# Kernel tuning notes

Measured on AMD Instinct MI355X. Metric: run time of the kernel, lower is better.

The kernel has to match this reference:

```python
import jax, jax.numpy as jnp
import numpy as np

HID = 1024
INTER = 4096
NUM_EXPERTS = 4096
NUM_KEYS = 64  # floor(sqrt(4096))
TOP_K = 8
B, S = 2, 2048


def setup_inputs() -> dict:
    key = jax.random.key(0)
    ks = jax.random.split(key, 7)
    sc = 0.02
    return {
        "hidden_states": jax.random.normal(ks[0], (B, S, HID), jnp.float32),
        "w_gate": jax.random.normal(ks[1], (INTER, HID), jnp.float32) * sc,
        "w_up": jax.random.normal(ks[2], (INTER, HID), jnp.float32) * sc,
        "w_down": jax.random.normal(ks[3], (HID, INTER), jnp.float32) * sc,
        "w_router": jax.random.normal(ks[4], (NUM_KEYS * 2, HID), jnp.float32) * sc,
        "down_embed": jax.random.normal(ks[5], (NUM_EXPERTS, HID), jnp.float32) * sc,
        "up_embed": jax.random.normal(ks[6], (NUM_EXPERTS, HID), jnp.float32) * sc,
    }


def reference(hidden_states, w_gate, w_up, w_down, w_router, down_embed, up_embed):
    b, s, h = hidden_states.shape
    n = b * s
    # router: [b,s,2*nk] -> row-major reshape to (2, n, nk), matching torch .view
    router_logits = (hidden_states @ w_router.T).reshape(2, n, NUM_KEYS)
    # topk with k == nk is a full descending sort (faithful to torch .topk)
    scores_xy, idx_xy = jax.lax.top_k(router_logits, NUM_KEYS)
    scores_x, scores_y = scores_xy[0], scores_xy[1]  # (n, nk) each
    idx_x, idx_y = idx_xy[0], idx_xy[1]
    all_scores = (scores_x[:, :, None] + scores_y[:, None, :]).reshape(n, NUM_KEYS * NUM_KEYS)
    all_indices = (idx_x[:, :, None] * NUM_KEYS + idx_y[:, None, :]).reshape(n, NUM_KEYS * NUM_KEYS)
    scores, pos = jax.lax.top_k(all_scores, TOP_K)  # (n, top_k)
    indices = jnp.take_along_axis(all_indices, pos, axis=-1)
    routing_weights = jax.nn.softmax(scores, axis=-1)
    routing_weights = routing_weights / routing_weights.sum(-1, keepdims=True)  # norm_topk_prob
    de = down_embed[indices]  # (n, top_k, h)
    ue = up_embed[indices]    # (n, top_k, h)
    x_flat = hidden_states.reshape(n, h)
    ew = jnp.einsum('nkh,nh->nk', de, x_flat)
    ew = jax.nn.silu(ew) * routing_weights
    experts_states = jnp.einsum('nk,nkh->nh', ew, ue).reshape(b, s, h)
    mlp = (jax.nn.silu(x_flat @ w_gate.T) * (x_flat @ w_up.T)) @ w_down.T
    out = mlp.reshape(b, s, h) + experts_states
    return (out, router_logits)
```

## Files before the change

### kernel.cpp

```cpp
#include <hip/hip_runtime.h>
#include <hip/hip_bf16.h>
#include <stdint.h>

typedef __bf16 bf16;
typedef __attribute__((ext_vector_type(8))) __bf16 bf16x8;
typedef __attribute__((ext_vector_type(4))) float f32x4;

static constexpr int kTok = 4096;
static constexpr int kHid = 1024;
static constexpr int kInter = 4096;

#define GLDS16(g, l)                                                \
  __builtin_amdgcn_global_load_lds(                                 \
      (const __attribute__((address_space(1))) void*)(g),           \
      (__attribute__((address_space(3))) void*)(l), 16, 0, 0)

__global__ void __launch_bounds__(256) k_cvt_all(
    const float* X, const float* Wg, const float* Wu, const float* Wd,
    const float* Wr, bf16* Xb, bf16* Wgb, bf16* Wub, bf16* Wdb, bf16* Wrb) {
  const float* src;
  bf16* dst;
  long n;
  switch (blockIdx.y) {
    case 0: src = X;  dst = Xb;  n = (long)kTok * kHid;   break;
    case 1: src = Wg; dst = Wgb; n = (long)kInter * kHid; break;
    case 2: src = Wu; dst = Wub; n = (long)kInter * kHid; break;
    case 3: src = Wd; dst = Wdb; n = (long)kHid * kInter; break;
    default: src = Wr; dst = Wrb; n = 128L * kHid;        break;
  }
  const long i = ((long)blockIdx.x * 256 + threadIdx.x) * 8;
  if (i >= n) return;
  const f32x4 a = *(const f32x4*)(src + i);
  const f32x4 b = *(const f32x4*)(src + i + 4);
  bf16x8 o;
#pragma unroll
  for (int k = 0; k < 4; ++k) { o[k] = (bf16)a[k]; o[4 + k] = (bf16)b[k]; }
  *(bf16x8*)(dst + i) = o;
}

__global__ void __launch_bounds__(256, 2) gemm_router(
    const bf16* A, const bf16* Bm, float* outF) {
  constexpr int K = kHid, N = 128;
  __shared__ bf16 sA[128 * 32];
  __shared__ bf16 sB[128 * 32];
  const int t = threadIdx.x;
  const int w = t >> 6;
  const int L = t & 63;
  const long m0 = (long)blockIdx.y * 128;
  const int zb = blockIdx.z * 256;
  const int wm = (w >> 1) * 64;
  const int wn = (w & 1) * 64;

  f32x4 acc[4][4];
  const f32x4 fzero = {0.f, 0.f, 0.f, 0.f};
#pragma unroll
  for (int i = 0; i < 4; ++i)
#pragma unroll
    for (int j = 0; j < 4; ++j) acc[i][j] = fzero;

  const int r0 = t >> 2;
  const int ko = (t & 3) * 8;
  const bf16* gA0 = A + (m0 + r0) * K + zb + ko;
  const bf16* gA1 = gA0 + (long)64 * K;
  const bf16* gB0 = Bm + (long)r0 * K + zb + ko;
  const bf16* gB1 = gB0 + (long)64 * K;
  bf16* lA0 = sA + w * 512;
  bf16* lA1 = sA + 2048 + w * 512;
  bf16* lB0 = sB + w * 512;
  bf16* lB1 = sB + 2048 + w * 512;

  const int la = L & 15;
  const int lk = (L >> 4) * 8;
  const bf16* sAr = sA + (wm + la) * 32 + lk;
  const bf16* sBr = sB + (wn + la) * 32 + lk;

  for (int kt = 0; kt < 8; ++kt) {
    const int k0 = kt << 5;
    GLDS16(gA0 + k0, lA0);
    GLDS16(gA1 + k0, lA1);
    GLDS16(gB0 + k0, lB0);
    GLDS16(gB1 + k0, lB1);
    __syncthreads();
    bf16x8 af[4], bfm[4];
#pragma unroll
    for (int i = 0; i < 4; ++i) {
      af[i] = *(const bf16x8*)(sAr + i * 16 * 32);
      bfm[i] = *(const bf16x8*)(sBr + i * 16 * 32);
    }
#pragma unroll
    for (int i = 0; i < 4; ++i)
#pragma unroll
      for (int j = 0; j < 4; ++j)
        acc[i][j] = __builtin_amdgcn_mfma_f32_16x16x32_bf16(af[i], bfm[j],
                                                            acc[i][j], 0, 0, 0);
    __syncthreads();
  }
  const long col0 = wn + la;
  const long row0 = m0 + wm + (L >> 4) * 4;
#pragma unroll
  for (int i = 0; i < 4; ++i)
#pragma unroll
    for (int j = 0; j < 4; ++j)
#pragma unroll
      for (int r = 0; r < 4; ++r)
        __hip_atomic_fetch_add(&outF[(row0 + i * 16 + r) * N + col0 + j * 16],
                               acc[i][j][r], __ATOMIC_RELAXED,
                               __HIP_MEMORY_SCOPE_AGENT);
}

__global__ void __launch_bounds__(256, 2) gemm_gu(
    const bf16* X, const bf16* Wg, const bf16* Wu, bf16* H) {
  constexpr int K = kHid, N = kInter;
  __shared__ bf16 sX[128 * 32];
  __shared__ bf16 sG[128 * 32];
  __shared__ bf16 sU[128 * 32];
  const int t = threadIdx.x;
  const int w = t >> 6;
  const int L = t & 63;
  const long m0 = (long)blockIdx.y * 128;
  const long n0 = (long)blockIdx.x * 128;
  const int wm = (w >> 1) * 64;
  const int wn = (w & 1) * 64;

  f32x4 accG[4][4], accU[4][4];
  const f32x4 fzero = {0.f, 0.f, 0.f, 0.f};
#pragma unroll
  for (int i = 0; i < 4; ++i)
#pragma unroll
    for (int j = 0; j < 4; ++j) { accG[i][j] = fzero; accU[i][j] = fzero; }

  const int r0 = t >> 2;
  const int ko = (t & 3) * 8;
  const bf16* gX0 = X + (m0 + r0) * K + ko;
  const bf16* gX1 = gX0 + (long)64 * K;
  const bf16* gG0 = Wg + (n0 + r0) * K + ko;
  const bf16* gG1 = gG0 + (long)64 * K;
  const bf16* gU0 = Wu + (n0 + r0) * K + ko;
  const bf16* gU1 = gU0 + (long)64 * K;
  bf16* lX0 = sX + w * 512;
  bf16* lX1 = sX + 2048 + w * 512;
  bf16* lG0 = sG + w * 512;
  bf16* lG1 = sG + 2048 + w * 512;
  bf16* lU0 = sU + w * 512;
  bf16* lU1 = sU + 2048 + w * 512;

  const int la = L & 15;
  const int lk = (L >> 4) * 8;
  const bf16* sXr = sX + (wm + la) * 32 + lk;
  const bf16* sGr = sG + (wn + la) * 32 + lk;
  const bf16* sUr = sU + (wn + la) * 32 + lk;

  for (int kt = 0; kt < K / 32; ++kt) {
    const int k0 = kt << 5;
    GLDS16(gX0 + k0, lX0);
    GLDS16(gX1 + k0, lX1);
    GLDS16(gG0 + k0, lG0);
    GLDS16(gG1 + k0, lG1);
    GLDS16(gU0 + k0, lU0);
    GLDS16(gU1 + k0, lU1);
    __syncthreads();
    bf16x8 af[4], bg[4], bu[4];
#pragma unroll
    for (int i = 0; i < 4; ++i) {
      af[i] = *(const bf16x8*)(sXr + i * 16 * 32);
      bg[i] = *(const bf16x8*)(sGr + i * 16 * 32);
      bu[i] = *(const bf16x8*)(sUr + i * 16 * 32);
    }
#pragma unroll
    for (int i = 0; i < 4; ++i)
#pragma unroll
      for (int j = 0; j < 4; ++j) {
        accG[i][j] = __builtin_amdgcn_mfma_f32_16x16x32_bf16(af[i], bg[j],
                                                             accG[i][j], 0, 0, 0);
        accU[i][j] = __builtin_amdgcn_mfma_f32_16x16x32_bf16(af[i], bu[j],
                                                             accU[i][j], 0, 0, 0);
      }
    __syncthreads();
  }
  const long col0 = n0 + wn + la;
  const long row0 = m0 + wm + (L >> 4) * 4;
#pragma unroll
  for (int i = 0; i < 4; ++i)
#pragma unroll
    for (int j = 0; j < 4; ++j)
#pragma unroll
      for (int r = 0; r < 4; ++r) {
        const float g = accG[i][j][r];
        const float u = accU[i][j][r];
        H[(row0 + i * 16 + r) * N + col0 + j * 16] =
            (bf16)(g / (1.f + __expf(-g)) * u);
      }
}

__global__ void __launch_bounds__(256, 2) gemm_down(
    const bf16* Hs, const bf16* Wd, float* out0) {
  constexpr int K = kInter, N = kHid;
  __shared__ bf16 sA[128 * 32];
  __shared__ bf16 sB[128 * 32];
  const int t = threadIdx.x;
  const int w = t >> 6;
  const int L = t & 63;
  const long m0 = (long)blockIdx.y * 128;
  const long n0 = (long)blockIdx.x * 128;
  const long zb = (long)blockIdx.z * 2048;
  const int wm = (w >> 1) * 64;
  const int wn = (w & 1) * 64;

  f32x4 acc[4][4];
  const f32x4 fzero = {0.f, 0.f, 0.f, 0.f};
#pragma unroll
  for (int i = 0; i < 4; ++i)
#pragma unroll
    for (int j = 0; j < 4; ++j) acc[i][j] = fzero;

  const int r0 = t >> 2;
  const int ko = (t & 3) * 8;
  const bf16* gA0 = Hs + (m0 + r0) * K + zb + ko;
  const bf16* gA1 = gA0 + (long)64 * K;
  const bf16* gB0 = Wd + (n0 + r0) * K + zb + ko;
  const bf16* gB1 = gB0 + (long)64 * K;
  bf16* lA0 = sA + w * 512;
  bf16* lA1 = sA + 2048 + w * 512;
  bf16* lB0 = sB + w * 512;
  bf16* lB1 = sB + 2048 + w * 512;

  const int la = L & 15;
  const int lk = (L >> 4) * 8;
  const bf16* sAr = sA + (wm + la) * 32 + lk;
  const bf16* sBr = sB + (wn + la) * 32 + lk;

  for (int kt = 0; kt < 64; ++kt) {
    const int k0 = kt << 5;
    GLDS16(gA0 + k0, lA0);
    GLDS16(gA1 + k0, lA1);
    GLDS16(gB0 + k0, lB0);
    GLDS16(gB1 + k0, lB1);
    __syncthreads();
    bf16x8 af[4], bfm[4];
#pragma unroll
    for (int i = 0; i < 4; ++i) {
      af[i] = *(const bf16x8*)(sAr + i * 16 * 32);
      bfm[i] = *(const bf16x8*)(sBr + i * 16 * 32);
    }
#pragma unroll
    for (int i = 0; i < 4; ++i)
#pragma unroll
      for (int j = 0; j < 4; ++j)
        acc[i][j] = __builtin_amdgcn_mfma_f32_16x16x32_bf16(af[i], bfm[j],
                                                            acc[i][j], 0, 0, 0);
    __syncthreads();
  }
  const long col0 = n0 + wn + la;
  const long row0 = m0 + wm + (L >> 4) * 4;
#pragma unroll
  for (int i = 0; i < 4; ++i)
#pragma unroll
    for (int j = 0; j < 4; ++j)
#pragma unroll
      for (int r = 0; r < 4; ++r)
        __hip_atomic_fetch_add(
            &out0[(row0 + i * 16 + r) * N + col0 + j * 16], acc[i][j][r],
            __ATOMIC_RELAXED, __HIP_MEMORY_SCOPE_AGENT);
}

__global__ void k_zero4(float* p) {
  const long i = ((long)blockIdx.x * 256 + threadIdx.x) * 4;
  const f32x4 z = {0.f, 0.f, 0.f, 0.f};
  *(f32x4*)(p + i) = z;
}

__global__ void __launch_bounds__(256) route_expert(
    const float* logits, const float* X, const float* dE, const float* uE,
    float* out0) {
  __shared__ float s_vals[4][128];
  __shared__ int s_idx[4][128];
  const int w = threadIdx.x >> 6;
  const int L = threadIdx.x & 63;
  const int j = blockIdx.x * 4 + w;

  const int half = (j & 1) * 64;
  const int rx = j >> 1;
  const float vx = logits[(long)rx * 128 + half + L];
  const float vy = logits[(long)(2048 + rx) * 128 + half + L];

  int rkx = 0, rky = 0;
  for (int m = 0; m < 64; ++m) {
    const float mx = __shfl(vx, m);
    const float my = __shfl(vy, m);
    rkx += (mx > vx) || (mx == vx && m < L);
    rky += (my > vy) || (my == vy && m < L);
  }
  rkx &= 63;
  rky &= 63;
  s_vals[w][rkx] = vx;
  s_idx[w][rkx] = L;
  s_vals[w][64 + rky] = vy;
  s_idx[w][64 + rky] = L;
  __syncthreads();

  int p = 0, q = 0;
  const bool valid = (L < 20);
  if (L < 8)       { p = L;      q = 0; }
  else if (L < 12) { p = L - 8;  q = 1; }
  else if (L < 14) { p = L - 12; q = 2; }
  else if (L < 16) { p = L - 14; q = 3; }
  else if (L < 20) { p = 0;      q = L - 12; }
  const float kNegBig = -3.0e38f;
  float myv = valid ? (s_vals[w][p] + s_vals[w][64 + q]) : kNegBig;
  int mypos = valid ? (p * 64 + q) : 0x7fffffff;

  float topv[8];
  int tope[8];
#pragma unroll
  for (int r = 0; r < 8; ++r) {
    float bv = myv;
    int bp = mypos;
#pragma unroll
    for (int d = 32; d > 0; d >>= 1) {
      const float ov = __shfl_xor(bv, d);
      const int op = __shfl_xor(bp, d);
      if (ov > bv || (ov == bv && op < bp)) { bv = ov; bp = op; }
    }
    topv[r] = bv;
    const int pp = (bp >> 6) & 127, qq = bp & 63;
    tope[r] = (s_idx[w][pp] * 64 + s_idx[w][64 + qq]) & 4095;
    if (mypos == bp) myv = kNegBig;
  }

  float e[8], wsum = 0.f;
#pragma unroll
  for (int r = 0; r < 8; ++r) {
    e[r] = __expf(topv[r] - topv[0]);
    wsum += e[r];
  }
  const float winv = 1.f / wsum;

  const long xoff = (long)j * kHid + L * 16;
  float xv[16], acc[16];
#pragma unroll
  for (int v4 = 0; v4 < 4; ++v4) {
    const f32x4 xl = *(const f32x4*)(X + xoff + v4 * 4);
#pragma unroll
    for (int i = 0; i < 4; ++i) { xv[v4 * 4 + i] = xl[i]; acc[v4 * 4 + i] = 0.f; }
  }

  for (int r = 0; r < 8; ++r) {
    const long eo = (long)tope[r] * kHid + L * 16;
    float d = 0.f;
#pragma unroll
    for (int v4 = 0; v4 < 4; ++v4) {
      const f32x4 dl = *(const f32x4*)(dE + eo + v4 * 4);
#pragma unroll
      for (int i = 0; i < 4; ++i) d += dl[i] * xv[v4 * 4 + i];
    }
#pragma unroll
    for (int dd = 32; dd > 0; dd >>= 1) d += __shfl_xor(d, dd);
    const float ew = d / (1.f + __expf(-d)) * (e[r] * winv);
#pragma unroll
    for (int v4 = 0; v4 < 4; ++v4) {
      const f32x4 ul = *(const f32x4*)(uE + eo + v4 * 4);
#pragma unroll
      for (int i = 0; i < 4; ++i) acc[v4 * 4 + i] += ew * ul[i];
    }
  }

  float* po = out0 + xoff;
#pragma unroll
  for (int v4 = 0; v4 < 4; ++v4) {
    f32x4 ov = *(const f32x4*)(po + v4 * 4);
#pragma unroll
    for (int i = 0; i < 4; ++i) ov[i] += acc[v4 * 4 + i];
    *(f32x4*)(po + v4 * 4) = ov;
  }
}

extern "C" void kernel_launch(void* const* d_in, const int* in_sizes, int n_in,
                              void* d_out, int out_size, void* d_ws,
                              size_t ws_size, hipStream_t stream) {
  (void)in_sizes; (void)n_in; (void)out_size; (void)ws_size;
  const float* X  = (const float*)d_in[0];
  const float* Wg = (const float*)d_in[1];
  const float* Wu = (const float*)d_in[2];
  const float* Wd = (const float*)d_in[3];
  const float* Wr = (const float*)d_in[4];
  const float* dE = (const float*)d_in[5];
  const float* uE = (const float*)d_in[6];

  float* out0 = (float*)d_out;
  float* out1 = out0 + (size_t)kTok * kHid;

  bf16* wsH = (bf16*)d_ws;
  bf16* Wrb = wsH;
  bf16* Xb  = wsH + (size_t)kTok * kInter;
  bf16* Wgb = Xb  + (size_t)kTok * kHid;
  bf16* Wub = Wgb + (size_t)kInter * kHid;
  bf16* Wdb = Wub + (size_t)kInter * kHid;

  dim3 blk(256);
  k_zero4<<<dim3((kTok * kHid + 2 * kTok * 64) / 1024), blk, 0, stream>>>(out0);
  k_cvt_all<<<dim3(2048, 5), blk, 0, stream>>>(X, Wg, Wu, Wd, Wr,
                                               Xb, Wgb, Wub, Wdb, Wrb);
  gemm_router<<<dim3(1, 32, 4), blk, 0, stream>>>(Xb, Wrb, out1);
  gemm_gu<<<dim3(32, 32), blk, 0, stream>>>(Xb, Wgb, Wub, wsH);
  gemm_down<<<dim3(8, 32, 2), blk, 0, stream>>>(wsH, Wdb, out0);
  route_expert<<<dim3(kTok / 4), blk, 0, stream>>>(out1, X, dE, uE, out0);
}
```

Baseline: 346.6 us.

## Multi-stage LDS pipelining in GEMMs and fuse output zeroing into conversion kernel

Reworks the router, gate/up and down GEMMs from a single-buffer load/sync/compute loop into a 3- or 4-deep LDS ring. Asynchronous global-to-LDS loads for future k-tiles are issued ahead and gated by vmcnt waits plus a barrier, and MFMA blocks are bracketed with s_setprio. This is meant to hide global memory latency behind MFMA work and remove one of the two barriers per k-step. Separately, the output-zeroing kernel is folded into the conversion kernel as an extra grid row, saving a launch. The cost is more LDS per block: gate/up uses 72KB and may lose the intended 2-blocks-per-CU occupancy. The hand-written vmcnt counts must also match the exact number of loads in flight.

```diff
diff --git a/kernel.cpp b/kernel.cpp
--- a/kernel.cpp
+++ b/kernel.cpp
@@ -15,9 +15,24 @@
       (const __attribute__((address_space(1))) void*)(g),           \
       (__attribute__((address_space(3))) void*)(l), 16, 0, 0)
 
+#define WAIT_BAR(N)                                     \
+  asm volatile("s_waitcnt vmcnt(" #N ")" ::: "memory"); \
+  __builtin_amdgcn_s_barrier();                         \
+  __builtin_amdgcn_sched_barrier(0)
+
 __global__ void __launch_bounds__(256) k_cvt_all(
     const float* X, const float* Wg, const float* Wu, const float* Wd,
-    const float* Wr, bf16* Xb, bf16* Wgb, bf16* Wub, bf16* Wdb, bf16* Wrb) {
+    const float* Wr, bf16* Xb, bf16* Wgb, bf16* Wub, bf16* Wdb, bf16* Wrb,
+    float* out0) {
+  const long i = ((long)blockIdx.x * 256 + threadIdx.x) * 8;
+  if (blockIdx.y == 5) {
+    if (i < (long)kTok * kHid + 2L * kTok * 64) {
+      const f32x4 z = {0.f, 0.f, 0.f, 0.f};
+      *(f32x4*)(out0 + i) = z;
+      *(f32x4*)(out0 + i + 4) = z;
+    }
+    return;
+  }
   const float* src;
   bf16* dst;
   long n;
@@ -28,7 +43,6 @@
     case 3: src = Wd; dst = Wdb; n = (long)kHid * kInter; break;
     default: src = Wr; dst = Wrb; n = 128L * kHid;        break;
   }
-  const long i = ((long)blockIdx.x * 256 + threadIdx.x) * 8;
   if (i >= n) return;
   const f32x4 a = *(const f32x4*)(src + i);
   const f32x4 b = *(const f32x4*)(src + i + 4);
@@ -41,8 +55,9 @@
 __global__ void __launch_bounds__(256, 2) gemm_router(
     const bf16* A, const bf16* Bm, float* outF) {
   constexpr int K = kHid, N = 128;
-  __shared__ bf16 sA[128 * 32];
-  __shared__ bf16 sB[128 * 32];
+  constexpr int NT = 8;
+  __shared__ bf16 sA[4][128 * 32];
+  __shared__ bf16 sB[4][128 * 32];
   const int t = threadIdx.x;
   const int w = t >> 6;
   const int L = t & 63;
@@ -64,37 +79,50 @@
   const bf16* gA1 = gA0 + (long)64 * K;
   const bf16* gB0 = Bm + (long)r0 * K + zb + ko;
   const bf16* gB1 = gB0 + (long)64 * K;
-  bf16* lA0 = sA + w * 512;
-  bf16* lA1 = sA + 2048 + w * 512;
-  bf16* lB0 = sB + w * 512;
-  bf16* lB1 = sB + 2048 + w * 512;
+  const int lo = w * 512;
+
+#define STAGE_R(b_, tt)                          \
+  {                                              \
+    const long kk_ = (long)(tt) << 5;            \
+    GLDS16(gA0 + kk_, &sA[b_][lo]);              \
+    GLDS16(gA1 + kk_, &sA[b_][2048 + lo]);       \
+    GLDS16(gB0 + kk_, &sB[b_][lo]);              \
+    GLDS16(gB1 + kk_, &sB[b_][2048 + lo]);       \
+  }
+  STAGE_R(0, 0); STAGE_R(1, 1); STAGE_R(2, 2);
 
   const int la = L & 15;
   const int lk = (L >> 4) * 8;
-  const bf16* sAr = sA + (wm + la) * 32 + lk;
-  const bf16* sBr = sB + (wn + la) * 32 + lk;
-
-  for (int kt = 0; kt < 8; ++kt) {
-    const int k0 = kt << 5;
-    GLDS16(gA0 + k0, lA0);
-    GLDS16(gA1 + k0, lA1);
-    GLDS16(gB0 + k0, lB0);
-    GLDS16(gB1 + k0, lB1);
-    __syncthreads();
-    bf16x8 af[4], bfm[4];
-#pragma unroll
-    for (int i = 0; i < 4; ++i) {
-      af[i] = *(const bf16x8*)(sAr + i * 16 * 32);
-      bfm[i] = *(const bf16x8*)(sBr + i * 16 * 32);
-    }
-#pragma unroll
-    for (int i = 0; i < 4; ++i)
-#pragma unroll
-      for (int j = 0; j < 4; ++j)
-        acc[i][j] = __builtin_amdgcn_mfma_f32_16x16x32_bf16(af[i], bfm[j],
-                                                            acc[i][j], 0, 0, 0);
-    __syncthreads();
-  }
+  const int roA = (wm + la) * 32 + lk;
+  const int roB = (wn + la) * 32 + lk;
+
+#define R_BODY(BUF)                                                         \
+  {                                                                         \
+    const bf16* pa = &sA[BUF][roA];                                         \
+    const bf16* pb = &sB[BUF][roB];                                         \
+    bf16x8 af[4], bfm[4];                                                   \
+    _Pragma("unroll") for (int i = 0; i < 4; ++i) {                         \
+      af[i] = *(const bf16x8*)(pa + i * 512);                               \
+      bfm[i] = *(const bf16x8*)(pb + i * 512);                              \
+    }                                                                       \
+    __builtin_amdgcn_s_setprio(1);                                          \
+    _Pragma("unroll") for (int i = 0; i < 4; ++i)                           \
+      _Pragma("unroll") for (int j = 0; j < 4; ++j)                         \
+        acc[i][j] = __builtin_amdgcn_mfma_f32_16x16x32_bf16(                \
+            af[i], bfm[j], acc[i][j], 0, 0, 0);                             \
+    __builtin_amdgcn_s_setprio(0);                                          \
+  }
+
+  for (int kt = 0; kt < NT - 2; ++kt) {
+    WAIT_BAR(8);
+    if (kt + 3 < NT) STAGE_R((kt + 3) & 3, kt + 3);
+    R_BODY(kt & 3);
+  }
+  WAIT_BAR(4);
+  R_BODY((NT - 2) & 3);
+  WAIT_BAR(0);
+  R_BODY((NT - 1) & 3);
+
   const long col0 = wn + la;
   const long row0 = m0 + wm + (L >> 4) * 4;
 #pragma unroll
@@ -111,9 +139,10 @@
 __global__ void __launch_bounds__(256, 2) gemm_gu(
     const bf16* X, const bf16* Wg, const bf16* Wu, bf16* H) {
   constexpr int K = kHid, N = kInter;
-  __shared__ bf16 sX[128 * 32];
-  __shared__ bf16 sG[128 * 32];
-  __shared__ bf16 sU[128 * 32];
+  constexpr int NT = K / 32;
+  __shared__ bf16 sX[3][128 * 32];
+  __shared__ bf16 sG[3][128 * 32];
+  __shared__ bf16 sU[3][128 * 32];
   const int t = threadIdx.x;
   const int w = t >> 6;
   const int L = t & 63;
@@ -137,46 +166,58 @@
   const bf16* gG1 = gG0 + (long)64 * K;
   const bf16* gU0 = Wu + (n0 + r0) * K + ko;
   const bf16* gU1 = gU0 + (long)64 * K;
-  bf16* lX0 = sX + w * 512;
-  bf16* lX1 = sX + 2048 + w * 512;
-  bf16* lG0 = sG + w * 512;
-  bf16* lG1 = sG + 2048 + w * 512;
-  bf16* lU0 = sU + w * 512;
-  bf16* lU1 = sU + 2048 + w * 512;
+  const int lo = w * 512;
+
+#define STAGE_GU(b_, tt)                         \
+  {                                              \
+    const long kk_ = (long)(tt) << 5;            \
+    GLDS16(gX0 + kk_, &sX[b_][lo]);              \
+    GLDS16(gX1 + kk_, &sX[b_][2048 + lo]);       \
+    GLDS16(gG0 + kk_, &sG[b_][lo]);              \
+    GLDS16(gG1 + kk_, &sG[b_][2048 + lo]);       \
+    GLDS16(gU0 + kk_, &sU[b_][lo]);              \
+    GLDS16(gU1 + kk_, &sU[b_][2048 + lo]);       \
+  }
+  STAGE_GU(0, 0); STAGE_GU(1, 1);
 
   const int la = L & 15;
   const int lk = (L >> 4) * 8;
-  const bf16* sXr = sX + (wm + la) * 32 + lk;
-  const bf16* sGr = sG + (wn + la) * 32 + lk;
-  const bf16* sUr = sU + (wn + la) * 32 + lk;
-
-  for (int kt = 0; kt < K / 32; ++kt) {
-    const int k0 = kt << 5;
-    GLDS16(gX0 + k0, lX0);
-    GLDS16(gX1 + k0, lX1);
-    GLDS16(gG0 + k0, lG0);
-    GLDS16(gG1 + k0, lG1);
-    GLDS16(gU0 + k0, lU0);
-    GLDS16(gU1 + k0, lU1);
-    __syncthreads();
-    bf16x8 af[4], bg[4], bu[4];
-#pragma unroll
-    for (int i = 0; i < 4; ++i) {
-      af[i] = *(const bf16x8*)(sXr + i * 16 * 32);
-      bg[i] = *(const bf16x8*)(sGr + i * 16 * 32);
-      bu[i] = *(const bf16x8*)(sUr + i * 16 * 32);
-    }
-#pragma unroll
-    for (int i = 0; i < 4; ++i)
-#pragma unroll
-      for (int j = 0; j < 4; ++j) {
-        accG[i][j] = __builtin_amdgcn_mfma_f32_16x16x32_bf16(af[i], bg[j],
-                                                             accG[i][j], 0, 0, 0);
-        accU[i][j] = __builtin_amdgcn_mfma_f32_16x16x32_bf16(af[i], bu[j],
-                                                             accU[i][j], 0, 0, 0);
-      }
-    __syncthreads();
-  }
+  const int roX = (wm + la) * 32 + lk;
+  const int roW = (wn + la) * 32 + lk;
+
+#define GU_BODY(BUF)                                                        \
+  {                                                                         \
+    const bf16* px = &sX[BUF][roX];                                         \
+    const bf16* pg = &sG[BUF][roW];                                         \
+    const bf16* pu = &sU[BUF][roW];                                         \
+    bf16x8 af[4], bg[4], bu[4];                                             \
+    _Pragma("unroll") for (int i = 0; i < 4; ++i) {                         \
+      af[i] = *(const bf16x8*)(px + i * 512);                               \
+      bg[i] = *(const bf16x8*)(pg + i * 512);                               \
+      bu[i] = *(const bf16x8*)(pu + i * 512);                               \
+    }                                                                       \
+    __builtin_amdgcn_s_setprio(1);                                          \
+    _Pragma("unroll") for (int i = 0; i < 4; ++i)                           \
+      _Pragma("unroll") for (int j = 0; j < 4; ++j) {                       \
+        accG[i][j] = __builtin_amdgcn_mfma_f32_16x16x32_bf16(               \
+            af[i], bg[j], accG[i][j], 0, 0, 0);                             \
+        accU[i][j] = __builtin_amdgcn_mfma_f32_16x16x32_bf16(               \
+            af[i], bu[j], accU[i][j], 0, 0, 0);                             \
+      }                                                                     \
+    __builtin_amdgcn_s_setprio(0);                                          \
+  }
+
+  int cur = 0;
+  for (int kt = 0; kt < NT - 1; ++kt) {
+    WAIT_BAR(6);
+    const int stg = (cur == 0) ? 2 : cur - 1;
+    if (kt + 2 < NT) STAGE_GU(stg, kt + 2);
+    GU_BODY(cur);
+    cur = (cur == 2) ? 0 : cur + 1;
+  }
+  WAIT_BAR(0);
+  GU_BODY(cur);
+
   const long col0 = n0 + wn + la;
   const long row0 = m0 + wm + (L >> 4) * 4;
 #pragma unroll
@@ -195,8 +236,9 @@
 __global__ void __launch_bounds__(256, 2) gemm_down(
     const bf16* Hs, const bf16* Wd, float* out0) {
   constexpr int K = kInter, N = kHid;
-  __shared__ bf16 sA[128 * 32];
-  __shared__ bf16 sB[128 * 32];
+  constexpr int NT = 64;
+  __shared__ bf16 sA[4][128 * 32];
+  __shared__ bf16 sB[4][128 * 32];
   const int t = threadIdx.x;
   const int w = t >> 6;
   const int L = t & 63;
@@ -219,37 +261,50 @@
   const bf16* gA1 = gA0 + (long)64 * K;
   const bf16* gB0 = Wd + (n0 + r0) * K + zb + ko;
   const bf16* gB1 = gB0 + (long)64 * K;
-  bf16* lA0 = sA + w * 512;
-  bf16* lA1 = sA + 2048 + w * 512;
-  bf16* lB0 = sB + w * 512;
-  bf16* lB1 = sB + 2048 + w * 512;
+  const int lo = w * 512;
+
+#define STAGE_D(b_, tt)                          \
+  {                                              \
+    const long kk_ = (long)(tt) << 5;            \
+    GLDS16(gA0 + kk_, &sA[b_][lo]);              \
+    GLDS16(gA1 + kk_, &sA[b_][2048 + lo]);       \
+    GLDS16(gB0 + kk_, &sB[b_][lo]);              \
+    GLDS16(gB1 + kk_, &sB[b_][2048 + lo]);       \
+  }
+  STAGE_D(0, 0); STAGE_D(1, 1); STAGE_D(2, 2);
 
   const int la = L & 15;
   const int lk = (L >> 4) * 8;
-  const bf16* sAr = sA + (wm + la) * 32 + lk;
-  const bf16* sBr = sB + (wn + la) * 32 + lk;
-
-  for (int kt = 0; kt < 64; ++kt) {
-    const int k0 = kt << 5;
-    GLDS16(gA0 + k0, lA0);
-    GLDS16(gA1 + k0, lA1);
-    GLDS16(gB0 + k0, lB0);
-    GLDS16(gB1 + k0, lB1);
-    __syncthreads();
-    bf16x8 af[4], bfm[4];
-#pragma unroll
-    for (int i = 0; i < 4; ++i) {
-      af[i] = *(const bf16x8*)(sAr + i * 16 * 32);
-      bfm[i] = *(const bf16x8*)(sBr + i * 16 * 32);
-    }
-#pragma unroll
-    for (int i = 0; i < 4; ++i)
-#pragma unroll
-      for (int j = 0; j < 4; ++j)
-        acc[i][j] = __builtin_amdgcn_mfma_f32_16x16x32_bf16(af[i], bfm[j],
-                                                            acc[i][j], 0, 0, 0);
-    __syncthreads();
-  }
+  const int roA = (wm + la) * 32 + lk;
+  const int roB = (wn + la) * 32 + lk;
+
+#define D_BODY(BUF)                                                         \
+  {                                                                         \
+    const bf16* pa = &sA[BUF][roA];                                         \
+    const bf16* pb = &sB[BUF][roB];                                         \
+    bf16x8 af[4], bfm[4];                                                   \
+    _Pragma("unroll") for (int i = 0; i < 4; ++i) {                         \
+      af[i] = *(const bf16x8*)(pa + i * 512);                               \
+      bfm[i] = *(const bf16x8*)(pb + i * 512);                              \
+    }                                                                       \
+    __builtin_amdgcn_s_setprio(1);                                          \
+    _Pragma("unroll") for (int i = 0; i < 4; ++i)                           \
+      _Pragma("unroll") for (int j = 0; j < 4; ++j)                         \
+        acc[i][j] = __builtin_amdgcn_mfma_f32_16x16x32_bf16(                \
+            af[i], bfm[j], acc[i][j], 0, 0, 0);                             \
+    __builtin_amdgcn_s_setprio(0);                                          \
+  }
+
+  for (int kt = 0; kt < NT - 2; ++kt) {
+    WAIT_BAR(8);
+    if (kt + 3 < NT) STAGE_D((kt + 3) & 3, kt + 3);
+    D_BODY(kt & 3);
+  }
+  WAIT_BAR(4);
+  D_BODY((NT - 2) & 3);
+  WAIT_BAR(0);
+  D_BODY((NT - 1) & 3);
+
   const long col0 = n0 + wn + la;
   const long row0 = m0 + wm + (L >> 4) * 4;
 #pragma unroll
@@ -261,12 +316,6 @@
         __hip_atomic_fetch_add(
             &out0[(row0 + i * 16 + r) * N + col0 + j * 16], acc[i][j][r],
             __ATOMIC_RELAXED, __HIP_MEMORY_SCOPE_AGENT);
-}
-
-__global__ void k_zero4(float* p) {
-  const long i = ((long)blockIdx.x * 256 + threadIdx.x) * 4;
-  const f32x4 z = {0.f, 0.f, 0.f, 0.f};
-  *(f32x4*)(p + i) = z;
 }
 
 __global__ void __launch_bounds__(256) route_expert(
@@ -397,9 +446,8 @@
   bf16* Wdb = Wub + (size_t)kInter * kHid;
 
   dim3 blk(256);
-  k_zero4<<<dim3((kTok * kHid + 2 * kTok * 64) / 1024), blk, 0, stream>>>(out0);
-  k_cvt_all<<<dim3(2048, 5), blk, 0, stream>>>(X, Wg, Wu, Wd, Wr,
-                                               Xb, Wgb, Wub, Wdb, Wrb);
+  k_cvt_all<<<dim3(2304, 6), blk, 0, stream>>>(X, Wg, Wu, Wd, Wr,
+                                               Xb, Wgb, Wub, Wdb, Wrb, out0);
   gemm_router<<<dim3(1, 32, 4), blk, 0, stream>>>(Xb, Wrb, out1);
   gemm_gu<<<dim3(32, 32), blk, 0, stream>>>(Xb, Wgb, Wub, wsH);
   gemm_down<<<dim3(8, 32, 2), blk, 0, stream>>>(wsH, Wdb, out0);
```

Result: no change. 345.1 us (-0.4%).

## Fuse router into gate-up GEMM and expert routing into down-projection launch

Applied to the files above, without the earlier changes.

The zeroing kernel is folded into the conversion kernel. The router GEMM now runs as an extra column of blocks in the gate/up GEMM, reading fp32 inputs directly with a full K loop, so it no longer needs atomics or separate zeroing. The down GEMM uses a 4-way K split and shares one launch with the routing/expert blocks, which now add their result with atomics. The gate/up tile is narrowed to 64 columns to raise occupancy. This cuts kernel launches and serialization but adds more atomic traffic. There is also a risk that routing blocks read the router logits before they are final, though the prior launch should complete first.

```diff
diff --git a/kernel.cpp b/kernel.cpp
--- a/kernel.cpp
+++ b/kernel.cpp
@@ -17,7 +17,16 @@
 
 __global__ void __launch_bounds__(256) k_cvt_all(
     const float* X, const float* Wg, const float* Wu, const float* Wd,
-    const float* Wr, bf16* Xb, bf16* Wgb, bf16* Wub, bf16* Wdb, bf16* Wrb) {
+    bf16* Xb, bf16* Wgb, bf16* Wub, bf16* Wdb, float* out0) {
+  const long i = ((long)blockIdx.x * 256 + threadIdx.x) * 8;
+  if (blockIdx.y == 4) {
+    if (i < (long)kTok * kHid) {
+      const f32x4 z = {0.f, 0.f, 0.f, 0.f};
+      *(f32x4*)(out0 + i) = z;
+      *(f32x4*)(out0 + i + 4) = z;
+    }
+    return;
+  }
   const float* src;
   bf16* dst;
   long n;
@@ -25,10 +34,8 @@
     case 0: src = X;  dst = Xb;  n = (long)kTok * kHid;   break;
     case 1: src = Wg; dst = Wgb; n = (long)kInter * kHid; break;
     case 2: src = Wu; dst = Wub; n = (long)kInter * kHid; break;
-    case 3: src = Wd; dst = Wdb; n = (long)kHid * kInter; break;
-    default: src = Wr; dst = Wrb; n = 128L * kHid;        break;
-  }
-  const long i = ((long)blockIdx.x * 256 + threadIdx.x) * 8;
+    default: src = Wd; dst = Wdb; n = (long)kHid * kInter; break;
+  }
   if (i >= n) return;
   const f32x4 a = *(const f32x4*)(src + i);
   const f32x4 b = *(const f32x4*)(src + i + 4);
@@ -38,245 +45,239 @@
   *(bf16x8*)(dst + i) = o;
 }
 
-__global__ void __launch_bounds__(256, 2) gemm_router(
-    const bf16* A, const bf16* Bm, float* outF) {
-  constexpr int K = kHid, N = 128;
-  __shared__ bf16 sA[128 * 32];
-  __shared__ bf16 sB[128 * 32];
+__global__ void __launch_bounds__(256, 3) gemm_gu_rt(
+    const bf16* X, const bf16* Wg, const bf16* Wu,
+    const float* Xf, const float* Wr, bf16* H, float* out1) {
+  __shared__ bf16 smem[8192];
   const int t = threadIdx.x;
   const int w = t >> 6;
   const int L = t & 63;
+  const int la = L & 15;
+  const int lk = (L >> 4) * 8;
+  const f32x4 fzero = {0.f, 0.f, 0.f, 0.f};
+
+  if (blockIdx.x == 64) {
+    bf16* sA = smem;
+    bf16* sB = smem + 4096;
+    const long m0 = (long)blockIdx.y * 128;
+    const int wm = (w >> 1) * 64;
+    const int wn = (w & 1) * 64;
+    f32x4 acc[4][4];
+#pragma unroll
+    for (int i = 0; i < 4; ++i)
+#pragma unroll
+      for (int j = 0; j < 4; ++j) acc[i][j] = fzero;
+
+    const int c0 = t, c1 = t + 256;
+    const long ar0 = m0 + (c0 >> 2), ar1 = m0 + (c1 >> 2);
+    const long br0 = (c0 >> 2), br1 = (c1 >> 2);
+    const int ko = (c0 & 3) * 8;
+    const bf16* sAr = sA + (wm + la) * 32 + lk;
+    const bf16* sBr = sB + (wn + la) * 32 + lk;
+
+    for (int kt = 0; kt < 32; ++kt) {
+      const long k0 = (long)kt << 5;
+      bf16x8 av0, av1, bv0, bv1;
+      {
+        const f32x4 x0 = *(const f32x4*)(Xf + ar0 * kHid + k0 + ko);
+        const f32x4 x1 = *(const f32x4*)(Xf + ar0 * kHid + k0 + ko + 4);
+        const f32x4 y0 = *(const f32x4*)(Xf + ar1 * kHid + k0 + ko);
+        const f32x4 y1 = *(const f32x4*)(Xf + ar1 * kHid + k0 + ko + 4);
+        const f32x4 p0 = *(const f32x4*)(Wr + br0 * kHid + k0 + ko);
+        const f32x4 p1 = *(const f32x4*)(Wr + br0 * kHid + k0 + ko + 4);
+        const f32x4 q0 = *(const f32x4*)(Wr + br1 * kHid + k0 + ko);
+        const f32x4 q1 = *(const f32x4*)(Wr + br1 * kHid + k0 + ko + 4);
+#pragma unroll
+        for (int i = 0; i < 4; ++i) {
+          av0[i] = (bf16)x0[i]; av0[4 + i] = (bf16)x1[i];
+          av1[i] = (bf16)y0[i]; av1[4 + i] = (bf16)y1[i];
+          bv0[i] = (bf16)p0[i]; bv0[4 + i] = (bf16)p1[i];
+          bv1[i] = (bf16)q0[i]; bv1[4 + i] = (bf16)q1[i];
+        }
+      }
+      __syncthreads();
+      *(bf16x8*)(sA + c0 * 8) = av0;
+      *(bf16x8*)(sA + c1 * 8) = av1;
+      *(bf16x8*)(sB + c0 * 8) = bv0;
+      *(bf16x8*)(sB + c1 * 8) = bv1;
+      __syncthreads();
+      bf16x8 af[4], bfm[4];
+#pragma unroll
+      for (int i = 0; i < 4; ++i) {
+        af[i] = *(const bf16x8*)(sAr + i * 512);
+        bfm[i] = *(const bf16x8*)(sBr + i * 512);
+      }
+#pragma unroll
+      for (int i = 0; i < 4; ++i)
+#pragma unroll
+        for (int j = 0; j < 4; ++j)
+          acc[i][j] = __builtin_amdgcn_mfma_f32_16x16x32_bf16(
+              af[i], bfm[j], acc[i][j], 0, 0, 0);
+    }
+    const long col0 = wn + la;
+    const long row0 = m0 + wm + (L >> 4) * 4;
+#pragma unroll
+    for (int i = 0; i < 4; ++i)
+#pragma unroll
+      for (int j = 0; j < 4; ++j)
+#pragma unroll
+        for (int r = 0; r < 4; ++r)
+          out1[(row0 + i * 16 + r) * 128 + col0 + j * 16] = acc[i][j][r];
+    return;
+  }
+
+  bf16* sX = smem;
+  bf16* sG = smem + 4096;
+  bf16* sU = sG + 2048;
   const long m0 = (long)blockIdx.y * 128;
-  const int zb = blockIdx.z * 256;
+  const long n0 = (long)blockIdx.x * 64;
   const int wm = (w >> 1) * 64;
-  const int wn = (w & 1) * 64;
-
-  f32x4 acc[4][4];
-  const f32x4 fzero = {0.f, 0.f, 0.f, 0.f};
+  const int wn = (w & 1) * 32;
+
+  f32x4 accG[4][2], accU[4][2];
 #pragma unroll
   for (int i = 0; i < 4; ++i)
 #pragma unroll
-    for (int j = 0; j < 4; ++j) acc[i][j] = fzero;
+    for (int j = 0; j < 2; ++j) { accG[i][j] = fzero; accU[i][j] = fzero; }
 
   const int r0 = t >> 2;
   const int ko = (t & 3) * 8;
-  const bf16* gA0 = A + (m0 + r0) * K + zb + ko;
-  const bf16* gA1 = gA0 + (long)64 * K;
-  const bf16* gB0 = Bm + (long)r0 * K + zb + ko;
-  const bf16* gB1 = gB0 + (long)64 * K;
-  bf16* lA0 = sA + w * 512;
-  bf16* lA1 = sA + 2048 + w * 512;
-  bf16* lB0 = sB + w * 512;
-  bf16* lB1 = sB + 2048 + w * 512;
-
-  const int la = L & 15;
-  const int lk = (L >> 4) * 8;
-  const bf16* sAr = sA + (wm + la) * 32 + lk;
-  const bf16* sBr = sB + (wn + la) * 32 + lk;
-
-  for (int kt = 0; kt < 8; ++kt) {
-    const int k0 = kt << 5;
-    GLDS16(gA0 + k0, lA0);
-    GLDS16(gA1 + k0, lA1);
-    GLDS16(gB0 + k0, lB0);
-    GLDS16(gB1 + k0, lB1);
+  const bf16* gX0 = X + (m0 + r0) * kHid + ko;
+  const bf16* gX1 = gX0 + (long)64 * kHid;
+  const bf16* gG0 = Wg + (n0 + r0) * kHid + ko;
+  const bf16* gU0 = Wu + (n0 + r0) * kHid + ko;
+  bf16* lX0 = sX + w * 512;
+  bf16* lX1 = sX + 2048 + w * 512;
+  bf16* lG = sG + w * 512;
+  bf16* lU = sU + w * 512;
+
+  const bf16* sXr = sX + (wm + la) * 32 + lk;
+  const bf16* sGr = sG + (wn + la) * 32 + lk;
+  const bf16* sUr = sU + (wn + la) * 32 + lk;
+
+  for (int kt = 0; kt < 32; ++kt) {
+    const long k0 = (long)kt << 5;
+    GLDS16(gX0 + k0, lX0);
+    GLDS16(gX1 + k0, lX1);
+    GLDS16(gG0 + k0, lG);
+    GLDS16(gU0 + k0, lU);
     __syncthreads();
-    bf16x8 af[4], bfm[4];
-#pragma unroll
-    for (int i = 0; i < 4; ++i) {
-      af[i] = *(const bf16x8*)(sAr + i * 16 * 32);
-      bfm[i] = *(const bf16x8*)(sBr + i * 16 * 32);
-    }
-#pragma unroll
-    for (int i = 0; i < 4; ++i)
-#pragma unroll
-      for (int j = 0; j < 4; ++j)
-        acc[i][j] = __builtin_amdgcn_mfma_f32_16x16x32_bf16(af[i], bfm[j],
-                                                            acc[i][j], 0, 0, 0);
+    bf16x8 af[4], bg[2], bu[2];
+#pragma unroll
+    for (int i = 0; i < 4; ++i) af[i] = *(const bf16x8*)(sXr + i * 512);
+#pragma unroll
+    for (int j = 0; j < 2; ++j) {
+      bg[j] = *(const bf16x8*)(sGr + j * 512);
+      bu[j] = *(const bf16x8*)(sUr + j * 512);
+    }
+#pragma unroll
+    for (int i = 0; i < 4; ++i)
+#pragma unroll
+      for (int j = 0; j < 2; ++j) {
+        accG[i][j] = __builtin_amdgcn_mfma_f32_16x16x32_bf16(
+            af[i], bg[j], accG[i][j], 0, 0, 0);
+        accU[i][j] = __builtin_amdgcn_mfma_f32_16x16x32_bf16(
+            af[i], bu[j], accU[i][j], 0, 0, 0);
+      }
     __syncthreads();
   }
-  const long col0 = wn + la;
+  const long col0 = n0 + wn + la;
   const long row0 = m0 + wm + (L >> 4) * 4;
 #pragma unroll
   for (int i = 0; i < 4; ++i)
 #pragma unroll
-    for (int j = 0; j < 4; ++j)
-#pragma unroll
-      for (int r = 0; r < 4; ++r)
-        __hip_atomic_fetch_add(&outF[(row0 + i * 16 + r) * N + col0 + j * 16],
-                               acc[i][j][r], __ATOMIC_RELAXED,
-                               __HIP_MEMORY_SCOPE_AGENT);
+    for (int j = 0; j < 2; ++j)
+#pragma unroll
+      for (int r = 0; r < 4; ++r) {
+        const float g = accG[i][j][r];
+        const float u = accU[i][j][r];
+        H[(row0 + i * 16 + r) * kInter + col0 + j * 16] =
+            (bf16)(g / (1.f + __expf(-g)) * u);
+      }
 }
 
-__global__ void __launch_bounds__(256, 2) gemm_gu(
-    const bf16* X, const bf16* Wg, const bf16* Wu, bf16* H) {
-  constexpr int K = kHid, N = kInter;
-  __shared__ bf16 sX[128 * 32];
-  __shared__ bf16 sG[128 * 32];
-  __shared__ bf16 sU[128 * 32];
+__global__ void __launch_bounds__(256, 3) gemm_down_re(
+    const bf16* Hs, const bf16* Wd, const float* logits, const float* Xf,
+    const float* dE, const float* uE, float* out0) {
+  __shared__ char smem[16384];
+  const int bid = blockIdx.x;
   const int t = threadIdx.x;
   const int w = t >> 6;
   const int L = t & 63;
-  const long m0 = (long)blockIdx.y * 128;
-  const long n0 = (long)blockIdx.x * 128;
-  const int wm = (w >> 1) * 64;
-  const int wn = (w & 1) * 64;
-
-  f32x4 accG[4][4], accU[4][4];
-  const f32x4 fzero = {0.f, 0.f, 0.f, 0.f};
-#pragma unroll
-  for (int i = 0; i < 4; ++i)
-#pragma unroll
-    for (int j = 0; j < 4; ++j) { accG[i][j] = fzero; accU[i][j] = fzero; }
-
-  const int r0 = t >> 2;
-  const int ko = (t & 3) * 8;
-  const bf16* gX0 = X + (m0 + r0) * K + ko;
-  const bf16* gX1 = gX0 + (long)64 * K;
-  const bf16* gG0 = Wg + (n0 + r0) * K + ko;
-  const bf16* gG1 = gG0 + (long)64 * K;
-  const bf16* gU0 = Wu + (n0 + r0) * K + ko;
-  const bf16* gU1 = gU0 + (long)64 * K;
-  bf16* lX0 = sX + w * 512;
-  bf16* lX1 = sX + 2048 + w * 512;
-  bf16* lG0 = sG + w * 512;
-  bf16* lG1 = sG + 2048 + w * 512;
-  bf16* lU0 = sU + w * 512;
-  bf16* lU1 = sU + 2048 + w * 512;
-
-  const int la = L & 15;
-  const int lk = (L >> 4) * 8;
-  const bf16* sXr = sX + (wm + la) * 32 + lk;
-  const bf16* sGr = sG + (wn + la) * 32 + lk;
-  const bf16* sUr = sU + (wn + la) * 32 + lk;
-
-  for (int kt = 0; kt < K / 32; ++kt) {
-    const int k0 = kt << 5;
-    GLDS16(gX0 + k0, lX0);
-    GLDS16(gX1 + k0, lX1);
-    GLDS16(gG0 + k0, lG0);
-    GLDS16(gG1 + k0, lG1);
-    GLDS16(gU0 + k0, lU0);
-    GLDS16(gU1 + k0, lU1);
-    __syncthreads();
-    bf16x8 af[4], bg[4], bu[4];
-#pragma unroll
-    for (int i = 0; i < 4; ++i) {
-      af[i] = *(const bf16x8*)(sXr + i * 16 * 32);
-      bg[i] = *(const bf16x8*)(sGr + i * 16 * 32);
-      bu[i] = *(const bf16x8*)(sUr + i * 16 * 32);
-    }
-#pragma unroll
-    for (int i = 0; i < 4; ++i)
-#pragma unroll
-      for (int j = 0; j < 4; ++j) {
-        accG[i][j] = __builtin_amdgcn_mfma_f32_16x16x32_bf16(af[i], bg[j],
-                                                             accG[i][j], 0, 0, 0);
-        accU[i][j] = __builtin_amdgcn_mfma_f32_16x16x32_bf16(af[i], bu[j],
-                                                             accU[i][j], 0, 0, 0);
+
+  if (bid < 1024) {
+    constexpr int K = kInter, N = kHid;
+    bf16* sA = (bf16*)smem;
+    bf16* sB = (bf16*)smem + 4096;
+    const int bx = bid & 7;
+    const int by = (bid >> 3) & 31;
+    const int bz = bid >> 8;
+    const long m0 = (long)by * 128;
+    const long n0 = (long)bx * 128;
+    const long zb = (long)bz * 1024;
+    const int wm = (w >> 1) * 64;
+    const int wn = (w & 1) * 64;
+    const int la = L & 15;
+    const int lk = (L >> 4) * 8;
+
+    f32x4 acc[4][4];
+    const f32x4 fzero = {0.f, 0.f, 0.f, 0.f};
+#pragma unroll
+    for (int i = 0; i < 4; ++i)
+#pragma unroll
+      for (int j = 0; j < 4; ++j) acc[i][j] = fzero;
+
+    const int r0 = t >> 2;
+    const int ko = (t & 3) * 8;
+    const bf16* gA0 = Hs + (m0 + r0) * K + zb + ko;
+    const bf16* gA1 = gA0 + (long)64 * K;
+    const bf16* gB0 = Wd + (n0 + r0) * K + zb + ko;
+    const bf16* gB1 = gB0 + (long)64 * K;
+    bf16* lA0 = sA + w * 512;
+    bf16* lA1 = sA + 2048 + w * 512;
+    bf16* lB0 = sB + w * 512;
+    bf16* lB1 = sB + 2048 + w * 512;
+    const bf16* sAr = sA + (wm + la) * 32 + lk;
+    const bf16* sBr = sB + (wn + la) * 32 + lk;
+
+    for (int kt = 0; kt < 32; ++kt) {
+      const long k0 = (long)kt << 5;
+      GLDS16(gA0 + k0, lA0);
+      GLDS16(gA1 + k0, lA1);
+      GLDS16(gB0 + k0, lB0);
+      GLDS16(gB1 + k0, lB1);
+      __syncthreads();
+      bf16x8 af[4], bfm[4];
+#pragma unroll
+      for (int i = 0; i < 4; ++i) {
+        af[i] = *(const bf16x8*)(sAr + i * 512);
+        bfm[i] = *(const bf16x8*)(sBr + i * 512);
       }
-    __syncthreads();
-  }
-  const long col0 = n0 + wn + la;
-  const long row0 = m0 + wm + (L >> 4) * 4;
-#pragma unroll
-  for (int i = 0; i < 4; ++i)
-#pragma unroll
-    for (int j = 0; j < 4; ++j)
-#pragma unroll
-      for (int r = 0; r < 4; ++r) {
-        const float g = accG[i][j][r];
-        const float u = accU[i][j][r];
-        H[(row0 + i * 16 + r) * N + col0 + j * 16] =
-            (bf16)(g / (1.f + __expf(-g)) * u);
-      }
-}
-
-__global__ void __launch_bounds__(256, 2) gemm_down(
-    const bf16* Hs, const bf16* Wd, float* out0) {
-  constexpr int K = kInter, N = kHid;
-  __shared__ bf16 sA[128 * 32];
-  __shared__ bf16 sB[128 * 32];
-  const int t = threadIdx.x;
-  const int w = t >> 6;
-  const int L = t & 63;
-  const long m0 = (long)blockIdx.y * 128;
-  const long n0 = (long)blockIdx.x * 128;
-  const long zb = (long)blockIdx.z * 2048;
-  const int wm = (w >> 1) * 64;
-  const int wn = (w & 1) * 64;
-
-  f32x4 acc[4][4];
-  const f32x4 fzero = {0.f, 0.f, 0.f, 0.f};
-#pragma unroll
-  for (int i = 0; i < 4; ++i)
-#pragma unroll
-    for (int j = 0; j < 4; ++j) acc[i][j] = fzero;
-
-  const int r0 = t >> 2;
-  const int ko = (t & 3) * 8;
-  const bf16* gA0 = Hs + (m0 + r0) * K + zb + ko;
-  const bf16* gA1 = gA0 + (long)64 * K;
-  const bf16* gB0 = Wd + (n0 + r0) * K + zb + ko;
-  const bf16* gB1 = gB0 + (long)64 * K;
-  bf16* lA0 = sA + w * 512;
-  bf16* lA1 = sA + 2048 + w * 512;
-  bf16* lB0 = sB + w * 512;
-  bf16* lB1 = sB + 2048 + w * 512;
-
-  const int la = L & 15;
-  const int lk = (L >> 4) * 8;
-  const bf16* sAr = sA + (wm + la) * 32 + lk;
-  const bf16* sBr = sB + (wn + la) * 32 + lk;
-
-  for (int kt = 0; kt < 64; ++kt) {
-    const int k0 = kt << 5;
-    GLDS16(gA0 + k0, lA0);
-    GLDS16(gA1 + k0, lA1);
-    GLDS16(gB0 + k0, lB0);
-    GLDS16(gB1 + k0, lB1);
-    __syncthreads();
-    bf16x8 af[4], bfm[4];
-#pragma unroll
-    for (int i = 0; i < 4; ++i) {
-      af[i] = *(const bf16x8*)(sAr + i * 16 * 32);
-      bfm[i] = *(const bf16x8*)(sBr + i * 16 * 32);
-    }
+#pragma unroll
+      for (int i = 0; i < 4; ++i)
+#pragma unroll
+        for (int j = 0; j < 4; ++j)
+          acc[i][j] = __builtin_amdgcn_mfma_f32_16x16x32_bf16(
+              af[i], bfm[j], acc[i][j], 0, 0, 0);
+      __syncthreads();
+    }
+    const long col0 = n0 + wn + la;
+    const long row0 = m0 + wm + (L >> 4) * 4;
 #pragma unroll
     for (int i = 0; i < 4; ++i)
 #pragma unroll
       for (int j = 0; j < 4; ++j)
-        acc[i][j] = __builtin_amdgcn_mfma_f32_16x16x32_bf16(af[i], bfm[j],
-                                                            acc[i][j], 0, 0, 0);
-    __syncthreads();
-  }
-  const long col0 = n0 + wn + la;
-  const long row0 = m0 + wm + (L >> 4) * 4;
-#pragma unroll
-  for (int i = 0; i < 4; ++i)
-#pragma unroll
-    for (int j = 0; j < 4; ++j)
-#pragma unroll
-      for (int r = 0; r < 4; ++r)
-        __hip_atomic_fetch_add(
-            &out0[(row0 + i * 16 + r) * N + col0 + j * 16], acc[i][j][r],
-            __ATOMIC_RELAXED, __HIP_MEMORY_SCOPE_AGENT);
-}
-
-__global__ void k_zero4(float* p) {
-  const long i = ((long)blockIdx.x * 256 + threadIdx.x) * 4;
-  const f32x4 z = {0.f, 0.f, 0.f, 0.f};
-  *(f32x4*)(p + i) = z;
-}
-
-__global__ void __launch_bounds__(256) route_expert(
-    const float* logits, const float* X, const float* dE, const float* uE,
-    float* out0) {
-  __shared__ float s_vals[4][128];
-  __shared__ int s_idx[4][128];
-  const int w = threadIdx.x >> 6;
-  const int L = threadIdx.x & 63;
-  const int j = blockIdx.x * 4 + w;
+#pragma unroll
+        for (int r = 0; r < 4; ++r)
+          __hip_atomic_fetch_add(
+              &out0[(row0 + i * 16 + r) * N + col0 + j * 16], acc[i][j][r],
+              __ATOMIC_RELAXED, __HIP_MEMORY_SCOPE_AGENT);
+    return;
+  }
+
+  float (*s_vals)[128] = (float (*)[128])smem;
+  int (*s_idx)[128] = (int (*)[128])(smem + 2048);
+  const int j = (bid - 1024) * 4 + w;
 
   const int half = (j & 1) * 64;
   const int rx = j >> 1;
@@ -339,7 +340,7 @@
   float xv[16], acc[16];
 #pragma unroll
   for (int v4 = 0; v4 < 4; ++v4) {
-    const f32x4 xl = *(const f32x4*)(X + xoff + v4 * 4);
+    const f32x4 xl = *(const f32x4*)(Xf + xoff + v4 * 4);
 #pragma unroll
     for (int i = 0; i < 4; ++i) { xv[v4 * 4 + i] = xl[i]; acc[v4 * 4 + i] = 0.f; }
   }
@@ -366,12 +367,11 @@
 
   float* po = out0 + xoff;
 #pragma unroll
-  for (int v4 = 0; v4 < 4; ++v4) {
-    f32x4 ov = *(const f32x4*)(po + v4 * 4);
-#pragma unroll
-    for (int i = 0; i < 4; ++i) ov[i] += acc[v4 * 4 + i];
-    *(f32x4*)(po + v4 * 4) = ov;
-  }
+  for (int v4 = 0; v4 < 4; ++v4)
+#pragma unroll
+    for (int i = 0; i < 4; ++i)
+      __hip_atomic_fetch_add(po + v4 * 4 + i, acc[v4 * 4 + i],
+                             __ATOMIC_RELAXED, __HIP_MEMORY_SCOPE_AGENT);
 }
 
 extern "C" void kernel_launch(void* const* d_in, const int* in_sizes, int n_in,
@@ -390,18 +390,14 @@
   float* out1 = out0 + (size_t)kTok * kHid;
 
   bf16* wsH = (bf16*)d_ws;
-  bf16* Wrb = wsH;
   bf16* Xb  = wsH + (size_t)kTok * kInter;
   bf16* Wgb = Xb  + (size_t)kTok * kHid;
   bf16* Wub = Wgb + (size_t)kInter * kHid;
   bf16* Wdb = Wub + (size_t)kInter * kHid;
 
   dim3 blk(256);
-  k_zero4<<<dim3((kTok * kHid + 2 * kTok * 64) / 1024), blk, 0, stream>>>(out0);
-  k_cvt_all<<<dim3(2048, 5), blk, 0, stream>>>(X, Wg, Wu, Wd, Wr,
-                                               Xb, Wgb, Wub, Wdb, Wrb);
-  gemm_router<<<dim3(1, 32, 4), blk, 0, stream>>>(Xb, Wrb, out1);
-  gemm_gu<<<dim3(32, 32), blk, 0, stream>>>(Xb, Wgb, Wub, wsH);
-  gemm_down<<<dim3(8, 32, 2), blk, 0, stream>>>(wsH, Wdb, out0);
-  route_expert<<<dim3(kTok / 4), blk, 0, stream>>>(out1, X, dE, uE, out0);
+  k_cvt_all<<<dim3(2048, 5), blk, 0, stream>>>(X, Wg, Wu, Wd,
+                                               Xb, Wgb, Wub, Wdb, out0);
+  gemm_gu_rt<<<dim3(65, 32), blk, 0, stream>>>(Xb, Wgb, Wub, X, Wr, wsH, out1);
+  gemm_down_re<<<dim3(2048), blk, 0, stream>>>(wsH, Wdb, out1, X, dE, uE, out0);
 }
```

New measurement: 563.1 us. 62.5% more time.
